# Performance work log

Measured on AMD Instinct MI355X. Metric: run time of the kernel, lower is better.

Reference implementation:

```python
import jax, jax.numpy as jnp
import numpy as np

B, L, D, H, S, E, FF = 4, 2048, 1024, 16, 512, 8, 4096
DH = D // H  # head dim = 64
EPS = 1e-5


def setup_inputs() -> dict:
    key = jax.random.key(0)
    ks = jax.random.split(key, 12)
    std = 0.02
    return {
        "x": jax.random.normal(ks[0], (B, L, D), jnp.float32),
        "slot_query": jax.random.normal(ks[1], (H, S, DH), jnp.float32) * std,
        "slot_key": jax.random.normal(ks[2], (H, S, DH), jnp.float32) * std,
        "w_dispatch_k": jax.random.normal(ks[3], (D, D), jnp.float32) * std,
        "w_dispatch_v": jax.random.normal(ks[4], (D, D), jnp.float32) * std,
        "w_combine_q": jax.random.normal(ks[5], (D, D), jnp.float32) * std,
        "w_in": jax.random.normal(ks[6], (E, FF, D), jnp.float32) * std,
        "b_in": jnp.zeros((E, FF), jnp.float32),
        "w_out": jax.random.normal(ks[7], (E, D, FF), jnp.float32) * std,
        "b_out": jnp.zeros((E, D), jnp.float32),
        "pre_norm_w": jnp.ones((D,), jnp.float32),
        "pre_norm_b": jnp.zeros((D,), jnp.float32),
    }


def _layer_norm(x, w, b, eps=EPS):
    m = jnp.mean(x, axis=-1, keepdims=True)
    v = jnp.mean(jnp.square(x - m), axis=-1, keepdims=True)
    return (x - m) * jax.lax.rsqrt(v + eps) * w + b


def _sdpa(q, k, v):
    # q: (..., Q, d), k: (..., K, d), v: (..., K, d)
    scale = 1.0 / np.sqrt(q.shape[-1])
    scores = jnp.einsum("...qd,...kd->...qk", q, k) * scale
    p = jax.nn.softmax(scores, axis=-1)
    return jnp.einsum("...qk,...kd->...qd", p, v)


def _split_heads(t):  # (B, N, D) -> (B, H, N, DH)
    b, n, _ = t.shape
    return t.reshape(b, n, H, DH).transpose(0, 2, 1, 3)


def _merge_heads(t):  # (B, H, N, DH) -> (B, N, D)
    b, h, n, d = t.shape
    return t.transpose(0, 2, 1, 3).reshape(b, n, h * d)


def reference(x, slot_query, slot_key, w_dispatch_k, w_dispatch_v, w_combine_q,
              w_in, b_in, w_out, b_out, pre_norm_w, pre_norm_b):
    # pre-norm
    xn = _layer_norm(x, pre_norm_w, pre_norm_b)

    # ---- dispatch: slots attend to tokens ----
    k = _split_heads(xn @ w_dispatch_k.T)        # (B,H,L,DH)
    v = _split_heads(xn @ w_dispatch_v.T)        # (B,H,L,DH)
    y = _sdpa(slot_query[None], k, v)            # (B,H,S,DH)
    y = _merge_heads(y)                          # (B,S,D)

    # ---- experts: batched per-expert MLP with relu^2 activation ----
    y = y.reshape(B, E, S // E, D)
    h = jnp.einsum("besd,efd->besf", y, w_in) + b_in[None, :, None, :]
    h = jnp.square(jax.nn.relu(h))               # relu2
    eo = jnp.einsum("besf,edf->besd", h, w_out) + b_out[None, :, None, :]
    eo = eo.reshape(B, S, D)

    # ---- combine: tokens attend to slots ----
    q = _split_heads(xn @ w_combine_q.T)         # (B,H,L,DH)
    vc = _split_heads(eo)                        # (B,H,S,DH)
    o = _sdpa(q, slot_key[None], vc)             # (B,H,L,DH)
    return _merge_heads(o)                       # (B,L,D)
```

## Files before the change

### kernel.cpp

```cpp
#include <hip/hip_runtime.h>
#include <hip/hip_bf16.h>

#define B_  4
#define L_  2048
#define D_  1024
#define H_  16
#define S_  512
#define E_  8
#define FF_ 4096
#define DH_ 64

typedef _Float16 half8 __attribute__((ext_vector_type(8)));
typedef _Float16 half4v __attribute__((ext_vector_type(4)));
typedef float floatx4 __attribute__((ext_vector_type(4)));
typedef unsigned short u16;

__device__ inline u16 f2h(float v) {
  _Float16 x = (_Float16)v;
  return __builtin_bit_cast(u16, x);
}

__device__ inline void gload_lds16(const void* g, void* l) {
  __builtin_amdgcn_global_load_lds(
      (const __attribute__((address_space(1))) void*)g,
      (__attribute__((address_space(3))) void*)l, 16, 0, 0);
}

__device__ inline int swz(int row, int colh) {
  return row * 64 + (colh ^ ((row & 7) << 3));
}
__device__ inline int swz1(int row, int colh) {
  return row * 64 + ((colh & ~7) ^ ((row & 7) << 3)) + (colh & 7);
}

__global__ __launch_bounds__(256) void ln_f16(const float* __restrict__ x,
    const float* __restrict__ w, const float* __restrict__ bb,
    u16* __restrict__ xn) {
  int row = blockIdx.x;
  int tid = threadIdx.x;
  float4 v = ((const float4*)(x + (long)row * D_))[tid];
  float s = v.x + v.y + v.z + v.w;
  __shared__ float red[4];
  #pragma unroll
  for (int off = 32; off > 0; off >>= 1) s += __shfl_down(s, off);
  int wid = tid >> 6, lane = tid & 63;
  if (lane == 0) red[wid] = s;
  __syncthreads();
  float mean = (red[0] + red[1] + red[2] + red[3]) * (1.0f / D_);
  __syncthreads();
  float dx = v.x - mean, dy = v.y - mean, dz = v.z - mean, dw = v.w - mean;
  float s2 = dx*dx + dy*dy + dz*dz + dw*dw;
  #pragma unroll
  for (int off = 32; off > 0; off >>= 1) s2 += __shfl_down(s2, off);
  if (lane == 0) red[wid] = s2;
  __syncthreads();
  float var = (red[0] + red[1] + red[2] + red[3]) * (1.0f / D_);
  float rstd = rsqrtf(var + 1e-5f);
  float4 wv = ((const float4*)w)[tid];
  float4 bv = ((const float4*)bb)[tid];
  half4v o = { (_Float16)(dx * rstd * wv.x + bv.x),
               (_Float16)(dy * rstd * wv.y + bv.y),
               (_Float16)(dz * rstd * wv.z + bv.z),
               (_Float16)(dw * rstd * wv.w + bv.w) };
  *(half4v*)&xn[(long)row * D_ + tid * 4] = o;
}

__global__ __launch_bounds__(256) void wcvt(const float* __restrict__ w0,
    const float* __restrict__ w1, const float* __restrict__ w2,
    const float* __restrict__ sq, const float* __restrict__ skq,
    u16* __restrict__ dst) {
  long i = ((long)blockIdx.x * 256 + threadIdx.x) * 8;
  const float* src; long off; float sc = 1.0f;
  if (i < 3145728) {
    int wsel = (int)(i >> 20);
    src = (wsel == 0) ? w0 : (wsel == 1) ? w1 : w2;
    off = i & 1048575;
  } else if (i < 3670016) {
    src = sq; off = i - 3145728; sc = 0.125f;
  } else {
    src = skq; off = i - 3670016;
  }
  float4 a = *(const float4*)(src + off);
  float4 b = *(const float4*)(src + off + 4);
  half8 h = { (_Float16)(a.x*sc), (_Float16)(a.y*sc), (_Float16)(a.z*sc), (_Float16)(a.w*sc),
              (_Float16)(b.x*sc), (_Float16)(b.y*sc), (_Float16)(b.z*sc), (_Float16)(b.w*sc) };
  *(half8*)(dst + i) = h;
}

__global__ __launch_bounds__(256) void proj_f16(
    const u16* __restrict__ A, const u16* __restrict__ Wc,
    u16* __restrict__ kh, u16* __restrict__ vT, u16* __restrict__ qh) {
  const int wsel = blockIdx.x >> 3;
  const int n0 = (blockIdx.x & 7) * 128, m0 = blockIdx.y * 128;
  const u16* Bh = Wc + (long)wsel * 1048576;
  const int tid = threadIdx.x, l = tid & 63, w = tid >> 6;
  const int wr = w >> 1, wc = w & 1;
  __shared__ __align__(16) u16 As[2][128 * 32];
  __shared__ __align__(16) u16 Bs[2][128 * 32];
  floatx4 acc[4][4] = {};

  const int ck = (l & 3) ^ ((l >> 3) & 3);
  const long gaA0 = (long)(m0 + w * 32 + (l >> 2)) * D_ + ck * 8;
  const long gaA1 = gaA0 + 16 * D_;
  const long gaB0 = (long)(n0 + w * 32 + (l >> 2)) * D_ + ck * 8;
  const long gaB1 = gaB0 + 16 * D_;

  #define PSTAGE(buf, kt)                                          \
    do {                                                           \
      gload_lds16(A + gaA0 + (kt), &As[buf][(w * 32) * 32]);       \
      gload_lds16(A + gaA1 + (kt), &As[buf][(w * 32 + 16) * 32]);  \
      gload_lds16(Bh + gaB0 + (kt), &Bs[buf][(w * 32) * 32]);      \
      gload_lds16(Bh + gaB1 + (kt), &Bs[buf][(w * 32 + 16) * 32]); \
    } while (0)

  PSTAGE(0, 0);
  __syncthreads();

  int cur = 0;
  const int q = l >> 4;
  for (int t = 0; t < 32; ++t) {
    if (t < 31) PSTAGE(cur ^ 1, (t + 1) * 32);
    half8 af[4], bfr[4];
    #pragma unroll
    for (int fr = 0; fr < 4; ++fr) {
      int row = wr * 64 + fr * 16 + (l & 15);
      af[fr] = *(const half8*)&As[cur][row * 32 + ((q ^ ((row >> 1) & 3)) << 3)];
    }
    #pragma unroll
    for (int fc = 0; fc < 4; ++fc) {
      int rr = wc * 64 + fc * 16 + (l & 15);
      bfr[fc] = *(const half8*)&Bs[cur][rr * 32 + ((q ^ ((rr >> 1) & 3)) << 3)];
    }
    #pragma unroll
    for (int fr = 0; fr < 4; ++fr)
      #pragma unroll
      for (int fc = 0; fc < 4; ++fc)
        acc[fr][fc] = __builtin_amdgcn_mfma_f32_16x16x32_f16(af[fr], bfr[fc], acc[fr][fc], 0, 0, 0);
    __syncthreads();
    cur ^= 1;
  }
  #undef PSTAGE

  if (wsel == 1) {
    #pragma unroll
    for (int fr = 0; fr < 4; ++fr)
      #pragma unroll
      for (int fc = 0; fc < 4; ++fc) {
        int row = m0 + wr * 64 + fr * 16 + (l >> 4) * 4;
        int col = n0 + wc * 64 + fc * 16 + (l & 15);
        half4v o = { (_Float16)acc[fr][fc][0], (_Float16)acc[fr][fc][1],
                     (_Float16)acc[fr][fc][2], (_Float16)acc[fr][fc][3] };
        long idx = ((long)(row >> 11) * 1024 + col) * 2048 + (row & 2047);
        *(half4v*)&vT[idx] = o;
      }
  } else {
    u16* C = (wsel == 0) ? kh : qh;
    const float sc = (wsel == 2) ? 0.125f : 1.0f;
    #pragma unroll
    for (int fr = 0; fr < 4; ++fr)
      #pragma unroll
      for (int fc = 0; fc < 4; ++fc)
        #pragma unroll
        for (int r = 0; r < 4; ++r) {
          int row = m0 + wr * 64 + fr * 16 + (l >> 4) * 4 + r;
          int col = n0 + wc * 64 + fc * 16 + (l & 15);
          C[(long)row * D_ + col] = f2h(acc[fr][fc][r] * sc);
        }
  }
}

template<int MODE>
__global__ __launch_bounds__(512) void expert_gemm(
    const u16* __restrict__ A, const float* __restrict__ Bw,
    const float* __restrict__ bias, u16* __restrict__ Ch,
    float* __restrict__ Cp) {
  constexpr int LDA = (MODE == 1) ? D_ : FF_;
  constexpr int LDB = (MODE == 1) ? D_ : FF_;
  const int e = blockIdx.z;
  const int n0 = blockIdx.x * 64;
  const int kc0 = (MODE == 2) ? blockIdx.y * 1024 : 0;
  const int tid = threadIdx.x, l = tid & 63, w = tid >> 6;
  const int wm = w >> 1, wn = w & 1;
  const int lr = l & 15, q = l >> 4;

  __shared__ __align__(16) u16  As[2][256 * 32];
  __shared__ __align__(16) float Bs[2][64 * 32];

  long asrc[2];
  #pragma unroll
  for (int i = 0; i < 2; ++i) {
    int ar = w * 32 + i * 16 + (l >> 2);
    long grow = (MODE == 1) ? ((long)(ar >> 6) * 512 + e * 64 + (ar & 63))
                            : (((long)(ar >> 6) * 8 + e) * 64 + (ar & 63));
    int ck = (l & 3) ^ (ar & 3);
    asrc[i] = grow * (long)LDA + kc0 + ck * 8;
  }
  const float* Bp = Bw + (long)e * (D_ * FF_);
  int brow = w * 8 + (l >> 3);
  int bck = (l & 7) ^ (brow & 7);
  long bsrc = (long)(n0 + brow) * LDB + kc0 + bck * 4;

  floatx4 acc[4][2] = {};

  #define STAGE(buf, kt)                                                 \
    do {                                                                 \
      gload_lds16(A + asrc[0] + (kt), &As[buf][(w * 32) * 32]);          \
      gload_lds16(A + asrc[1] + (kt), &As[buf][(w * 32 + 16) * 32]);     \
      gload_lds16(Bp + bsrc + (kt), &Bs[buf][(w * 8) * 32]);             \
    } while (0)

  STAGE(0, 0);
  __syncthreads();

  int cur = 0;
  for (int t = 0; t < 32; ++t) {
    if (t < 31) STAGE(cur ^ 1, (t + 1) * 32);
    half8 af[4];
    #pragma unroll
    for (int fr = 0; fr < 4; ++fr) {
      int row = wm * 64 + fr * 16 + lr;
      af[fr] = *(const half8*)&As[cur][row * 32 + ((q ^ (row & 3)) << 3)];
    }
    half8 bf[2];
    #pragma unroll
    for (int fc = 0; fc < 2; ++fc) {
      int rn = wn * 32 + fc * 16 + lr;
      float4 x0 = *(const float4*)&Bs[cur][rn * 32 + (((2 * q) ^ (rn & 7)) << 2)];
      float4 x1 = *(const float4*)&Bs[cur][rn * 32 + (((2 * q + 1) ^ (rn & 7)) << 2)];
      bf[fc] = (half8){ (_Float16)x0.x, (_Float16)x0.y, (_Float16)x0.z, (_Float16)x0.w,
                        (_Float16)x1.x, (_Float16)x1.y, (_Float16)x1.z, (_Float16)x1.w };
    }
    #pragma unroll
    for (int fr = 0; fr < 4; ++fr)
      #pragma unroll
      for (int fc = 0; fc < 2; ++fc)
        acc[fr][fc] = __builtin_amdgcn_mfma_f32_16x16x32_f16(af[fr], bf[fc], acc[fr][fc], 0, 0, 0);
    __syncthreads();
    cur ^= 1;
  }
  #undef STAGE

  #pragma unroll
  for (int fr = 0; fr < 4; ++fr)
    #pragma unroll
    for (int fc = 0; fc < 2; ++fc)
      #pragma unroll
      for (int r = 0; r < 4; ++r) {
        int ar = wm * 64 + fr * 16 + q * 4 + r;
        int col = n0 + wn * 32 + fc * 16 + lr;
        float val = acc[fr][fc][r];
        if constexpr (MODE == 1) {
          val += bias[e * FF_ + col];
          val = fmaxf(val, 0.f);
          val *= val;
          Ch[(((long)(ar >> 6) * 8 + e) * 64 + (ar & 63)) * FF_ + col] = f2h(val);
        } else {
          Cp[(((long)blockIdx.y * 8 + e) * 256 + ar) * 1024 + col] = val;
        }
      }
}

__global__ __launch_bounds__(256) void eo_reduce(const float* __restrict__ pb,
    const float* __restrict__ b_out, u16* __restrict__ eoT) {
  long j4 = (long)blockIdx.x * 256 + threadIdx.x;
  long j = j4 * 4;
  float4 s = ((const float4*)pb)[j4];
  #pragma unroll
  for (int c = 1; c < 4; ++c) {
    float4 t = ((const float4*)(pb + (long)c * 2097152))[j4];
    s.x += t.x; s.y += t.y; s.z += t.z; s.w += t.w;
  }
  int e = (int)(j >> 18);
  int rem = (int)(j & 262143);
  int row = rem >> 10, col = rem & 1023;
  float4 bv = *(const float4*)(b_out + e * 1024 + col);
  s.x += bv.x; s.y += bv.y; s.z += bv.z; s.w += bv.w;
  int b = row >> 6;
  int slot = e * 64 + (row & 63);
  float sv[4] = { s.x, s.y, s.z, s.w };
  #pragma unroll
  for (int i = 0; i < 4; ++i) {
    long idx = ((long)b * 1024 + col + i) * 512 + slot;
    eoT[idx] = f2h(sv[i]);
  }
}

template<bool OF32>
__global__ __launch_bounds__(256) void flash_f16(
    const u16* __restrict__ Qg, long qB, long qH, long qR,
    const u16* __restrict__ Kg, long kB, long kH, long kR,
    const u16* __restrict__ VTg, long vB, long vH, long vR,
    void* __restrict__ Og, long oB, long oH, long oR,
    float* __restrict__ pd, float* __restrict__ pacc,
    int Nq, int Nk, int nC) {
  __shared__ __align__(16) u16 Ks[64 * 64];
  __shared__ __align__(16) u16 Vt[64 * 64];
  const int tid = threadIdx.x, l = tid & 63, w = tid >> 6;
  const int g = l >> 4, lq = l & 15;
  const int bh = blockIdx.z, b = bh >> 4, hd = bh & 15;
  const int q0 = blockIdx.x * 64 + w * 16;
  const int chunk = Nk / nC, k0 = blockIdx.y * chunk;

  half8 qf[2];
  #pragma unroll
  for (int ks = 0; ks < 2; ++ks)
    qf[ks] = *(const half8*)(Qg + b * qB + hd * qH +
                             (long)(q0 + lq) * qR + ks * 32 + g * 8);

  const int srow = l >> 3;
  const int scol = ((l & 7) ^ srow) * 8;
  const long kbase = b * kB + hd * kH;
  const long vbase = b * vB + hd * vH;

  float lrun = 0.f;
  floatx4 o[4] = {};

  for (int t = 0; t < chunk; t += 64) {
    #pragma unroll
    for (int i = 0; i < 2; ++i) {
      int u = i * 4 + w;
      gload_lds16(Kg + kbase + (long)(k0 + t + u * 8 + srow) * kR + scol,
                  &Ks[u * 8 * 64]);
      gload_lds16(VTg + vbase + (long)(u * 8 + srow) * vR + k0 + t + scol,
                  &Vt[u * 8 * 64]);
    }
    __syncthreads();

    floatx4 s[4];
    #pragma unroll
    for (int j = 0; j < 4; ++j) s[j] = (floatx4){0.f, 0.f, 0.f, 0.f};
    #pragma unroll
    for (int ks = 0; ks < 2; ++ks)
      #pragma unroll
      for (int j = 0; j < 4; ++j) {
        half8 kf = *(const half8*)&Ks[swz(j * 16 + lq, ks * 32 + g * 8)];
        s[j] = __builtin_amdgcn_mfma_f32_16x16x32_f16(kf, qf[ks], s[j], 0, 0, 0);
      }

    half4v pa[4];
    float rs = 0.f;
    #pragma unroll
    for (int j = 0; j < 4; ++j)
      #pragma unroll
      for (int r = 0; r < 4; ++r) {
        float p = __expf(s[j][r]);
        rs += p;
        pa[j][r] = (_Float16)p;
      }
    lrun += rs;

    #pragma unroll
    for (int j = 0; j < 4; ++j)
      #pragma unroll
      for (int n = 0; n < 4; ++n) {
        half4v vf = *(const half4v*)&Vt[swz1(n * 16 + lq, j * 16 + g * 4)];
        o[n] = __builtin_amdgcn_mfma_f32_16x16x16f16(pa[j], vf, o[n], 0, 0, 0);
      }
    __syncthreads();
  }

  lrun += __shfl_xor(lrun, 16);
  lrun += __shfl_xor(lrun, 32);

  if (nC == 1) {
    float inv = 1.0f / lrun;
    float invr[4];
    #pragma unroll
    for (int r = 0; r < 4; ++r) invr[r] = __shfl(inv, g * 4 + r);
    #pragma unroll
    for (int n = 0; n < 4; ++n)
      #pragma unroll
      for (int r = 0; r < 4; ++r) {
        int row = q0 + g * 4 + r;
        int dh = n * 16 + lq;
        float val = o[n][r] * invr[r];
        long off = b * oB + hd * oH + (long)row * oR + dh;
        if (OF32) ((float*)Og)[off] = val;
        else      ((u16*)Og)[off] = f2h(val);
      }
  } else {
    if (l < 16) pd[((long)bh * Nq + q0 + l) * nC + blockIdx.y] = lrun;
    #pragma unroll
    for (int r = 0; r < 4; ++r) {
      int row = q0 + g * 4 + r;
      long idx = ((long)bh * Nq + row) * nC + blockIdx.y;
      #pragma unroll
      for (int n = 0; n < 4; ++n)
        pacc[idx * 64 + n * 16 + lq] = o[n][r];
    }
  }
}

__global__ __launch_bounds__(256) void finalize_f16(
    const float* __restrict__ pd, const float* __restrict__ pacc,
    u16* __restrict__ outp, int nC, int Nq, long oB, long oH, long oR) {
  int tid = threadIdx.x;
  int row = blockIdx.x * 4 + (tid >> 6);
  int lane = tid & 63;
  long base = (long)row * nC;
  float Dn = 0.f, a = 0.f;
  for (int c = 0; c < nC; ++c) {
    Dn += pd[base + c];
    a += pacc[(base + c) * 64 + lane];
  }
  int bh = row / Nq, qrow = row - bh * Nq;
  int b = bh >> 4, h = bh & 15;
  outp[(long)b * oB + (long)h * oH + (long)qrow * oR + lane] = f2h(a / Dn);
}

extern "C" void kernel_launch(void* const* d_in, const int* in_sizes, int n_in,
                              void* d_out, int out_size, void* d_ws, size_t ws_size,
                              hipStream_t stream) {
  const float* x     = (const float*)d_in[0];
  const float* sq    = (const float*)d_in[1];
  const float* skq   = (const float*)d_in[2];
  const float* wk    = (const float*)d_in[3];
  const float* wv    = (const float*)d_in[4];
  const float* wq    = (const float*)d_in[5];
  const float* w_in  = (const float*)d_in[6];
  const float* b_in  = (const float*)d_in[7];
  const float* w_out = (const float*)d_in[8];
  const float* b_out = (const float*)d_in[9];
  const float* pnw   = (const float*)d_in[10];
  const float* pnb   = (const float*)d_in[11];
  float* out = (float*)d_out;

  u16* ws   = (u16*)d_ws;
  u16* xnh  = ws;
  u16* kh   = xnh + 8388608;
  u16* vTh  = kh  + 8388608;
  u16* qh   = vTh + 8388608;
  u16* yh   = qh  + 8388608;
  u16* hh   = yh  + 2097152;
  u16* eoTh = hh  + 8388608;
  u16* wch  = eoTh + 2097152;
  u16* sqh  = wch + 3145728;
  u16* skh  = wch + 3670016;
  float* pbuf = (float*)(wch + 4194304);
  float* pdb  = pbuf + 8388608;
  float* pacc = pbuf;

  ln_f16<<<8192, 256, 0, stream>>>(x, pnw, pnb, xnh);
  wcvt<<<2048, 256, 0, stream>>>(wk, wv, wq, sq, skq, wch);

  proj_f16<<<dim3(24, 64, 1), 256, 0, stream>>>(xnh, wch, kh, vTh, qh);

  flash_f16<false><<<dim3(8, 4, 64), 256, 0, stream>>>(
      sqh, 0L, (long)(S_ * DH_), (long)DH_,
      kh, (long)(L_ * D_), (long)DH_, (long)D_,
      vTh, (long)(L_ * D_), (long)(DH_ * L_), (long)L_,
      nullptr, 0L, 0L, 0L,
      pdb, pacc, S_, L_, 4);
  finalize_f16<<<8192, 256, 0, stream>>>(pdb, pacc, yh, 4, S_,
      (long)(S_ * D_), (long)DH_, (long)D_);

  expert_gemm<1><<<dim3(64, 1, 8), 512, 0, stream>>>(yh, w_in, b_in, hh, nullptr);
  expert_gemm<2><<<dim3(16, 4, 8), 512, 0, stream>>>(hh, w_out, nullptr, nullptr, pbuf);
  eo_reduce<<<2048, 256, 0, stream>>>(pbuf, b_out, eoTh);

  flash_f16<true><<<dim3(32, 1, 64), 256, 0, stream>>>(
      qh, (long)(L_ * D_), (long)DH_, (long)D_,
      skh, 0L, (long)(S_ * DH_), (long)DH_,
      eoTh, (long)(S_ * D_), (long)(DH_ * S_), (long)S_,
      out, (long)(L_ * D_), (long)DH_, (long)D_,
      nullptr, nullptr, L_, S_, 1);
}
```

Before: 322.8 us.

## Rewrite projection GEMM with 256x256 tiles, 8 waves, and phased prefetch

The fused K/V/Q projection GEMM moves from 128x128 tiles with 4 waves and K-step 32 to 256x256 tiles with 8 waves and K-step 64. Global-to-LDS prefetch of the next stage is split into quarter chunks interleaved with four MFMA phases, using explicit vmcnt waits, barriers and s_setprio. The larger tile raises data reuse per LDS load and the finer interleave aims to hide load latency. The cost is 128KB of LDS per block, more accumulator registers, and only 384 blocks, which may limit occupancy.

```diff
diff --git a/kernel.cpp b/kernel.cpp
--- a/kernel.cpp
+++ b/kernel.cpp
@@ -87,67 +87,122 @@
   *(half8*)(dst + i) = h;
 }
 
-__global__ __launch_bounds__(256) void proj_f16(
+__global__ __launch_bounds__(512, 2) void proj8(
     const u16* __restrict__ A, const u16* __restrict__ Wc,
     u16* __restrict__ kh, u16* __restrict__ vT, u16* __restrict__ qh) {
-  const int wsel = blockIdx.x >> 3;
-  const int n0 = (blockIdx.x & 7) * 128, m0 = blockIdx.y * 128;
-  const u16* Bh = Wc + (long)wsel * 1048576;
+  const int nb = blockIdx.x & 3, wsel = blockIdx.x >> 2;
+  const int m0 = blockIdx.y * 256;
+  const int n0g = nb * 256;
   const int tid = threadIdx.x, l = tid & 63, w = tid >> 6;
-  const int wr = w >> 1, wc = w & 1;
-  __shared__ __align__(16) u16 As[2][128 * 32];
-  __shared__ __align__(16) u16 Bs[2][128 * 32];
-  floatx4 acc[4][4] = {};
-
-  const int ck = (l & 3) ^ ((l >> 3) & 3);
-  const long gaA0 = (long)(m0 + w * 32 + (l >> 2)) * D_ + ck * 8;
-  const long gaA1 = gaA0 + 16 * D_;
-  const long gaB0 = (long)(n0 + w * 32 + (l >> 2)) * D_ + ck * 8;
-  const long gaB1 = gaB0 + 16 * D_;
-
-  #define PSTAGE(buf, kt)                                          \
-    do {                                                           \
-      gload_lds16(A + gaA0 + (kt), &As[buf][(w * 32) * 32]);       \
-      gload_lds16(A + gaA1 + (kt), &As[buf][(w * 32 + 16) * 32]);  \
-      gload_lds16(Bh + gaB0 + (kt), &Bs[buf][(w * 32) * 32]);      \
-      gload_lds16(Bh + gaB1 + (kt), &Bs[buf][(w * 32 + 16) * 32]); \
+  const int wm = w >> 2, wn = w & 3;
+  const int lq = l & 15, g = l >> 4;
+
+  __shared__ __align__(16) u16 As[2][256 * 64];
+  __shared__ __align__(16) u16 Bs[2][256 * 64];
+
+  floatx4 acc[8][4] = {};
+
+  const int sch = ((l & 7) ^ (l >> 3)) * 8;
+  const long aoff = (long)(m0 + w * 16 + (l >> 3)) * 1024 + sch;
+  const long boff = (long)wsel * 1048576 +
+                    (long)(n0g + w * 16 + (l >> 3)) * 1024 + sch;
+  const int dA = w * 16 * 64;
+
+  #define STG_A(bb, kt, ha)                                                    \
+    do {                                                                       \
+      gload_lds16(A + aoff + (long)((ha) * 128) * 1024 + (kt) * 64,            \
+                  &As[bb][((ha) * 128) * 64 + dA]);                            \
+      gload_lds16(A + aoff + (long)((ha) * 128 + 8) * 1024 + (kt) * 64,        \
+                  &As[bb][((ha) * 128 + 8) * 64 + dA]);                        \
     } while (0)
-
-  PSTAGE(0, 0);
-  __syncthreads();
-
-  int cur = 0;
-  const int q = l >> 4;
-  for (int t = 0; t < 32; ++t) {
-    if (t < 31) PSTAGE(cur ^ 1, (t + 1) * 32);
-    half8 af[4], bfr[4];
-    #pragma unroll
-    for (int fr = 0; fr < 4; ++fr) {
-      int row = wr * 64 + fr * 16 + (l & 15);
-      af[fr] = *(const half8*)&As[cur][row * 32 + ((q ^ ((row >> 1) & 3)) << 3)];
-    }
-    #pragma unroll
-    for (int fc = 0; fc < 4; ++fc) {
-      int rr = wc * 64 + fc * 16 + (l & 15);
-      bfr[fc] = *(const half8*)&Bs[cur][rr * 32 + ((q ^ ((rr >> 1) & 3)) << 3)];
-    }
-    #pragma unroll
-    for (int fr = 0; fr < 4; ++fr)
-      #pragma unroll
-      for (int fc = 0; fc < 4; ++fc)
-        acc[fr][fc] = __builtin_amdgcn_mfma_f32_16x16x32_f16(af[fr], bfr[fc], acc[fr][fc], 0, 0, 0);
-    __syncthreads();
-    cur ^= 1;
-  }
-  #undef PSTAGE
+  #define STG_B(bb, kt, ha)                                                    \
+    do {                                                                       \
+      gload_lds16(Wc + boff + (long)((ha) * 128) * 1024 + (kt) * 64,           \
+                  &Bs[bb][((ha) * 128) * 64 + dA]);                            \
+      gload_lds16(Wc + boff + (long)((ha) * 128 + 8) * 1024 + (kt) * 64,       \
+                  &Bs[bb][((ha) * 128 + 8) * 64 + dA]);                        \
+    } while (0)
+
+  STG_A(0, 0, 0); STG_A(0, 0, 1); STG_B(0, 0, 0); STG_B(0, 0, 1);
+
+  for (int t = 0; t < 16; ++t) {
+    const int cur = t & 1, nxt = cur ^ 1;
+    const bool pf = (t < 15);
+
+    if (pf) {
+      STG_A(nxt, t + 1, 0);
+      asm volatile("s_waitcnt vmcnt(2)" ::: "memory");
+    } else {
+      asm volatile("s_waitcnt vmcnt(0)" ::: "memory");
+    }
+    __builtin_amdgcn_s_barrier();
+
+    half8 bf[4][2];
+    #pragma unroll
+    for (int fc = 0; fc < 4; ++fc)
+      #pragma unroll
+      for (int ks = 0; ks < 2; ++ks)
+        bf[fc][ks] = *(const half8*)&Bs[cur][(wn * 64 + fc * 16 + lq) * 64
+                                    + (((ks * 4 + g) ^ (lq & 7)) << 3)];
+    {
+      half8 af[2][2];
+      #pragma unroll
+      for (int i = 0; i < 2; ++i)
+        #pragma unroll
+        for (int ks = 0; ks < 2; ++ks)
+          af[i][ks] = *(const half8*)&As[cur][(wm * 128 + (0 * 2 + i) * 16 + lq) * 64
+                                      + (((ks * 4 + g) ^ (lq & 7)) << 3)];
+      __builtin_amdgcn_s_setprio(1);
+      #pragma unroll
+      for (int i = 0; i < 2; ++i)
+        #pragma unroll
+        for (int ks = 0; ks < 2; ++ks)
+          #pragma unroll
+          for (int fc = 0; fc < 4; ++fc)
+            acc[0 * 2 + i][fc] = __builtin_amdgcn_mfma_f32_16x16x32_f16(
+                af[i][ks], bf[fc][ks], acc[0 * 2 + i][fc], 0, 0, 0);
+      __builtin_amdgcn_s_setprio(0);
+    }
+    __builtin_amdgcn_s_barrier();
+
+    #define PHASE(p, STAGE_STMT)                                               \
+    {                                                                          \
+      half8 af[2][2];                                                          \
+      _Pragma("unroll")                                                        \
+      for (int i = 0; i < 2; ++i)                                              \
+        _Pragma("unroll")                                                      \
+        for (int ks = 0; ks < 2; ++ks)                                         \
+          af[i][ks] = *(const half8*)&As[cur][(wm * 128 + ((p) * 2 + i) * 16   \
+              + lq) * 64 + (((ks * 4 + g) ^ (lq & 7)) << 3)];                  \
+      if (pf) { STAGE_STMT; }                                                  \
+      __builtin_amdgcn_s_barrier();                                            \
+      __builtin_amdgcn_s_setprio(1);                                           \
+      _Pragma("unroll")                                                        \
+      for (int i = 0; i < 2; ++i)                                              \
+        _Pragma("unroll")                                                      \
+        for (int ks = 0; ks < 2; ++ks)                                         \
+          _Pragma("unroll")                                                    \
+          for (int fc = 0; fc < 4; ++fc)                                       \
+            acc[(p) * 2 + i][fc] = __builtin_amdgcn_mfma_f32_16x16x32_f16(     \
+                af[i][ks], bf[fc][ks], acc[(p) * 2 + i][fc], 0, 0, 0);         \
+      __builtin_amdgcn_s_setprio(0);                                           \
+      __builtin_amdgcn_s_barrier();                                            \
+    }
+    PHASE(1, STG_A(nxt, t + 1, 1))
+    PHASE(2, STG_B(nxt, t + 1, 0))
+    PHASE(3, STG_B(nxt, t + 1, 1))
+    #undef PHASE
+  }
+  #undef STG_A
+  #undef STG_B
 
   if (wsel == 1) {
     #pragma unroll
-    for (int fr = 0; fr < 4; ++fr)
+    for (int fr = 0; fr < 8; ++fr)
       #pragma unroll
       for (int fc = 0; fc < 4; ++fc) {
-        int row = m0 + wr * 64 + fr * 16 + (l >> 4) * 4;
-        int col = n0 + wc * 64 + fc * 16 + (l & 15);
+        int row = m0 + wm * 128 + fr * 16 + g * 4;
+        int col = n0g + wn * 64 + fc * 16 + lq;
         half4v o = { (_Float16)acc[fr][fc][0], (_Float16)acc[fr][fc][1],
                      (_Float16)acc[fr][fc][2], (_Float16)acc[fr][fc][3] };
         long idx = ((long)(row >> 11) * 1024 + col) * 2048 + (row & 2047);
@@ -157,14 +212,14 @@
     u16* C = (wsel == 0) ? kh : qh;
     const float sc = (wsel == 2) ? 0.125f : 1.0f;
     #pragma unroll
-    for (int fr = 0; fr < 4; ++fr)
+    for (int fr = 0; fr < 8; ++fr)
       #pragma unroll
       for (int fc = 0; fc < 4; ++fc)
         #pragma unroll
         for (int r = 0; r < 4; ++r) {
-          int row = m0 + wr * 64 + fr * 16 + (l >> 4) * 4 + r;
-          int col = n0 + wc * 64 + fc * 16 + (l & 15);
-          C[(long)row * D_ + col] = f2h(acc[fr][fc][r] * sc);
+          int row = m0 + wm * 128 + fr * 16 + g * 4 + r;
+          int col = n0g + wn * 64 + fc * 16 + lq;
+          C[(long)row * 1024 + col] = f2h(acc[fr][fc][r] * sc);
         }
   }
 }
@@ -443,7 +498,7 @@
   ln_f16<<<8192, 256, 0, stream>>>(x, pnw, pnb, xnh);
   wcvt<<<2048, 256, 0, stream>>>(wk, wv, wq, sq, skq, wch);
 
-  proj_f16<<<dim3(24, 64, 1), 256, 0, stream>>>(xnh, wch, kh, vTh, qh);
+  proj8<<<dim3(12, 32, 1), 512, 0, stream>>>(xnh, wch, kh, vTh, qh);
 
   flash_f16<false><<<dim3(8, 4, 64), 256, 0, stream>>>(
       sqh, 0L, (long)(S_ * DH_), (long)DH_,
```

Result: no change. 322.7 us (-0.0%).
